# Kernel tuning notes

Hardware: AMD Instinct MI355X
Metric: run time of the kernel (lower is better)

The kernel has to match this reference:

```python
import jax, jax.numpy as jnp
import numpy as np

NUM_HEADS = 16

def setup_inputs() -> dict:
    key = jax.random.key(0)
    k1, k2, k3 = jax.random.split(key, 3)
    B, S, H = 2, 2048, 1024
    hidden_states = jax.random.normal(k1, (B, S, H), dtype=jnp.float32)
    # nn.Linear default init scale ~ 1/sqrt(fan_in); keep magnitudes sane
    w_qkv = jax.random.normal(k2, (3 * H, H), dtype=jnp.float32) * (1.0 / np.sqrt(H))
    w_o = jax.random.normal(k3, (H, H), dtype=jnp.float32) * (1.0 / np.sqrt(H))
    return {"hidden_states": hidden_states, "w_qkv": w_qkv, "w_o": w_o}

def reference(hidden_states, w_qkv, w_o):
    B, S, H = hidden_states.shape
    nh = NUM_HEADS
    hd = H // nh
    scale = 1.0 / np.sqrt(hd)
    # fused QKV projection: [B,S,3H]
    qkv = jnp.einsum('bsh,oh->bso', hidden_states, w_qkv)
    qkv = qkv.reshape(B, S, 3, nh, hd)
    q = qkv[:, :, 0].transpose(0, 2, 1, 3)  # [B, nh, S, hd]
    k = qkv[:, :, 1].transpose(0, 2, 1, 3)
    v = qkv[:, :, 2].transpose(0, 2, 1, 3)
    # scaled dot-product attention (math identical to the online-softmax path)
    scores = jnp.einsum('bhqd,bhkd->bhqk', q, k) * scale
    probs = jax.nn.softmax(scores, axis=-1)
    attn = jnp.einsum('bhqk,bhkd->bhqd', probs, v)  # [B, nh, S, hd]
    attn = attn.transpose(0, 2, 1, 3).reshape(B, S, H)
    out = jnp.einsum('bsh,oh->bso', attn, w_o)
    return out
```

## Files before the change

kernel.cpp:

```cpp
#include <hip/hip_runtime.h>

using f32x4 = __attribute__((ext_vector_type(4))) float;
using s16x8 = __attribute__((ext_vector_type(8))) short;
using u16x8 = __attribute__((ext_vector_type(8))) unsigned short;
using u16x4 = __attribute__((ext_vector_type(4))) unsigned short;
using u32x2 = __attribute__((ext_vector_type(2))) unsigned int;

__device__ __forceinline__ unsigned short f2bf(float f) {
  union { float f; unsigned u; } v; v.f = f;
  return (unsigned short)((v.u + 0x7FFFu + ((v.u >> 16) & 1u)) >> 16);
}

__device__ __forceinline__ unsigned pk2bf(float a, float b) {
#if __has_builtin(__builtin_amdgcn_cvt_pk_bf16_f32)
  typedef __bf16 bf2 __attribute__((ext_vector_type(2)));
  union { bf2 v; unsigned u; } c;
  c.v = __builtin_amdgcn_cvt_pk_bf16_f32(a, b);
  return c.u;
#else
  return (unsigned)f2bf(a) | ((unsigned)f2bf(b) << 16);
#endif
}

__device__ __forceinline__ f32x4 fzero4() {
  f32x4 z; z[0] = 0.f; z[1] = 0.f; z[2] = 0.f; z[3] = 0.f; return z;
}

__device__ __forceinline__ void gl_lds16(const void* g, void* l) {
  __builtin_amdgcn_global_load_lds(
      (const __attribute__((address_space(1))) unsigned int*)g,
      (__attribute__((address_space(3))) unsigned int*)l, 16, 0, 0);
}

__global__ __launch_bounds__(256) void cvt_bf16(const float* __restrict__ h,
                                                const float* __restrict__ wq,
                                                const float* __restrict__ wo,
                                                unsigned short* __restrict__ dst) {
  const int blk = blockIdx.x;
  const float* src;
  if (blk < 2048) src = h;
  else if (blk < 3584) src = wq - 4194304;
  else src = wo - (4194304 + 3145728);
  const size_t i = (size_t)blk * 2048 + threadIdx.x * 8;
  f32x4 a0 = *(const f32x4*)(src + i);
  f32x4 a1 = *(const f32x4*)(src + i + 4);
  u32x2 v0, v1;
  v0[0] = pk2bf(a0[0], a0[1]); v0[1] = pk2bf(a0[2], a0[3]);
  v1[0] = pk2bf(a1[0], a1[1]); v1[1] = pk2bf(a1[2], a1[3]);
  *(u32x2*)(dst + i) = v0;
  *(u32x2*)(dst + i + 4) = v1;
}

template <int CMODE>
__global__ __launch_bounds__(256) void gemm_bt(const unsigned short* __restrict__ A,
                                               const unsigned short* __restrict__ B,
                                               void* __restrict__ Cp,
                                               void* __restrict__ Vgp,
                                               int M, int N, int K) {
  __shared__ unsigned short As[128 * 64];
  __shared__ unsigned short Bs[128 * 64];
  const int t = threadIdx.x;
  const int lane = t & 63, wid = t >> 6;
  const int l15 = lane & 15, quad = lane >> 4;
  const int bm = blockIdx.x * 128, bn = blockIdx.y * 128;
  const int wm = (wid >> 1) * 64, wn = (wid & 1) * 64;
  const int wbase = t & ~63;

  f32x4 acc[4][4];
#pragma unroll
  for (int i = 0; i < 4; ++i)
#pragma unroll
    for (int j = 0; j < 4; ++j) acc[i][j] = fzero4();

  for (int k0 = 0; k0 < K; k0 += 64) {
    __syncthreads();
#pragma unroll
    for (int i = 0; i < 4; ++i) {
      const int dc = t + i * 256;
      const int row = dc >> 3, cp = dc & 7;
      const int cl = cp ^ (row & 7);
      gl_lds16(A + (size_t)(bm + row) * K + k0 + cl * 8, &As[(size_t)(i * 256 + wbase) * 8]);
      gl_lds16(B + (size_t)(bn + row) * K + k0 + cl * 8, &Bs[(size_t)(i * 256 + wbase) * 8]);
    }
    __syncthreads();
#pragma unroll
    for (int c = 0; c < 2; ++c) {
      s16x8 af[4], bf[4];
#pragma unroll
      for (int mt = 0; mt < 4; ++mt) {
        const int row = wm + mt * 16 + l15;
        af[mt] = *(const s16x8*)&As[row * 64 + (((c * 4 + quad) ^ (l15 & 7)) * 8)];
      }
#pragma unroll
      for (int nt = 0; nt < 4; ++nt) {
        const int row = wn + nt * 16 + l15;
        bf[nt] = *(const s16x8*)&Bs[row * 64 + (((c * 4 + quad) ^ (l15 & 7)) * 8)];
      }
#pragma unroll
      for (int mt = 0; mt < 4; ++mt)
#pragma unroll
        for (int nt = 0; nt < 4; ++nt)
          acc[mt][nt] = __builtin_amdgcn_mfma_f32_16x16x32_bf16(af[mt], bf[nt], acc[mt][nt], 0, 0, 0);
    }
  }

  if (CMODE == 2 && bn >= 2048) {
#pragma unroll
    for (int mt = 0; mt < 4; ++mt)
#pragma unroll
      for (int nt = 0; nt < 4; ++nt) {
        const int row0 = bm + wm + mt * 16 + quad * 4;
        const int c = bn + wn + nt * 16 + l15 - 2048;
        const int b = row0 >> 11, s = row0 & 2047;
        u32x2 ov;
        ov[0] = pk2bf(acc[mt][nt][0], acc[mt][nt][1]);
        ov[1] = pk2bf(acc[mt][nt][2], acc[mt][nt][3]);
        *(u32x2*)&((unsigned short*)Vgp)[(size_t)b * (1024 * 2048) + (size_t)c * 2048 + s] = ov;
      }
    return;
  }

  const float qscale = (CMODE == 2 && bn < 1024) ? 0.18033688011112042f : 1.0f;
#pragma unroll
  for (int mt = 0; mt < 4; ++mt)
#pragma unroll
    for (int nt = 0; nt < 4; ++nt)
#pragma unroll
      for (int r = 0; r < 4; ++r) {
        const int row = bm + wm + mt * 16 + quad * 4 + r;
        const int col = bn + wn + nt * 16 + l15;
        if (CMODE == 0)
          ((float*)Cp)[(size_t)row * N + col] = acc[mt][nt][r];
        else
          ((unsigned short*)Cp)[(size_t)row * 2048 + col] = f2bf(acc[mt][nt][r] * qscale);
      }
}

__global__ __launch_bounds__(256) void fattn(const unsigned short* __restrict__ qk,
                                             const unsigned short* __restrict__ vg,
                                             unsigned short* __restrict__ attn) {
  constexpr int S = 2048, H = 1024, LD = 2048, HD = 64;
  __shared__ unsigned short smemKP[64 * 136];
  __shared__ unsigned short Vt[64 * 128];
  unsigned short* Ks = smemKP;
  unsigned short(*Pn)[136] = (unsigned short(*)[136])smemKP;

  const int t = threadIdx.x, lane = t & 63, wid = t >> 6;
  const int l15 = lane & 15, quad = lane >> 4;
  const int qt = blockIdx.x, h = blockIdx.y, b = blockIdx.z;
  const unsigned short* qbase = qk + (size_t)b * S * LD;
  const unsigned short* vbase = vg + ((size_t)b * 16 + h) * HD * S;
  const int qrow0 = qt * 64;
  const int wbase = t & ~63;

  s16x8 qf[2];
#pragma unroll
  for (int c = 0; c < 2; ++c)
    qf[c] = *(const s16x8*)(qbase + (size_t)(qrow0 + wid * 16 + l15) * LD +
                            h * HD + c * 32 + quad * 8);

  s16x8 ones;
#pragma unroll
  for (int j = 0; j < 8; ++j) ones[j] = (short)0x3F80;

  f32x4 o[4], lacc = fzero4();
#pragma unroll
  for (int i = 0; i < 4; ++i) o[i] = fzero4();

  for (int kt = 0; kt < S / 128; ++kt) {
    __syncthreads();
#pragma unroll
    for (int i = 0; i < 4; ++i) {
      const int pos = t + i * 256;
      {
        const int row = pos >> 3, s = pos & 7;
        const int clog = s ^ (row & 7);
        gl_lds16(qbase + (size_t)(kt * 128 + row) * LD + 1024 + h * HD + clog * 8,
                 &Ks[(size_t)(i * 256 + wbase) * 8]);
      }
      {
        const int row = pos >> 4, s = pos & 15;
        const int clog = s ^ (row & 7);
        gl_lds16(vbase + (size_t)row * S + kt * 128 + clog * 8,
                 &Vt[(size_t)(i * 256 + wbase) * 8]);
      }
    }
    __syncthreads();

    f32x4 st[8];
#pragma unroll
    for (int i = 0; i < 8; ++i) st[i] = fzero4();
#pragma unroll
    for (int c = 0; c < 2; ++c)
#pragma unroll
      for (int mt = 0; mt < 8; ++mt) {
        s16x8 kf = *(const s16x8*)&Ks[(mt * 16 + l15) * 64 + ((c * 4 + quad) ^ (l15 & 7)) * 8];
        st[mt] = __builtin_amdgcn_mfma_f32_16x16x32_bf16(kf, qf[c], st[mt], 0, 0, 0);
      }

#pragma unroll
    for (int mt = 0; mt < 8; ++mt)
#pragma unroll
      for (int r = 0; r < 4; ++r) st[mt][r] = __builtin_amdgcn_exp2f(st[mt][r]);

    __syncthreads();

#pragma unroll
    for (int mt = 0; mt < 8; ++mt) {
      u32x2 pk;
      pk[0] = pk2bf(st[mt][0], st[mt][1]);
      pk[1] = pk2bf(st[mt][2], st[mt][3]);
      *(u32x2*)&Pn[wid * 16 + l15][mt * 16 + quad * 4] = pk;
    }

#pragma unroll
    for (int c = 0; c < 4; ++c) {
      s16x8 pf = *(const s16x8*)&Pn[wid * 16 + l15][c * 32 + quad * 8];
      lacc = __builtin_amdgcn_mfma_f32_16x16x32_bf16(ones, pf, lacc, 0, 0, 0);
#pragma unroll
      for (int mt = 0; mt < 4; ++mt) {
        s16x8 vf = *(const s16x8*)&Vt[(mt * 16 + l15) * 128 + (((c * 4 + quad) ^ (l15 & 7))) * 8];
        o[mt] = __builtin_amdgcn_mfma_f32_16x16x32_bf16(vf, pf, o[mt], 0, 0, 0);
      }
    }
  }

  const float inv = 1.f / lacc[0];
  const int row = b * S + qrow0 + wid * 16 + l15;
#pragma unroll
  for (int mt = 0; mt < 4; ++mt) {
    u32x2 ov;
    ov[0] = pk2bf(o[mt][0] * inv, o[mt][1] * inv);
    ov[1] = pk2bf(o[mt][2] * inv, o[mt][3] * inv);
    *(u32x2*)&attn[(size_t)row * H + h * HD + mt * 16 + quad * 4] = ov;
  }
}

extern "C" void kernel_launch(void* const* d_in, const int* in_sizes, int n_in,
                              void* d_out, int out_size, void* d_ws, size_t ws_size,
                              hipStream_t stream) {
  const float* hidden = (const float*)d_in[0];
  const float* w_qkv = (const float*)d_in[1];
  const float* w_o = (const float*)d_in[2];
  float* out = (float*)d_out;

  constexpr int B = 2, S = 2048, H = 1024;
  constexpr int M = B * S;

  unsigned short* hbf = (unsigned short*)d_ws;
  unsigned short* wqbf = hbf + 4194304;
  unsigned short* wobf = wqbf + 3145728;
  unsigned short* qkbuf = wobf + 1048576;
  unsigned short* vg = qkbuf + (size_t)M * 2048;
  unsigned short* attn = hbf;

  dim3 blk(256);
  cvt_bf16<<<4096, blk, 0, stream>>>(hidden, w_qkv, w_o, hbf);
  gemm_bt<2><<<dim3(M / 128, (3 * H) / 128), blk, 0, stream>>>(
      hbf, wqbf, (void*)qkbuf, (void*)vg, M, 3 * H, H);
  fattn<<<dim3(S / 64, 16, B), blk, 0, stream>>>(qkbuf, vg, attn);
  gemm_bt<0><<<dim3(M / 128, H / 128), blk, 0, stream>>>(
      attn, wobf, (void*)out, nullptr, M, H, H);
}
```

Baseline: 206.1 us.

## Double-buffer K/V tiles and process 32 query rows per wave in attention

```diff
diff --git a/kernel.cpp b/kernel.cpp
--- a/kernel.cpp
+++ b/kernel.cpp
@@ -140,99 +140,127 @@
                                              const unsigned short* __restrict__ vg,
                                              unsigned short* __restrict__ attn) {
   constexpr int S = 2048, H = 1024, LD = 2048, HD = 64;
-  __shared__ unsigned short smemKP[64 * 136];
-  __shared__ unsigned short Vt[64 * 128];
-  unsigned short* Ks = smemKP;
-  unsigned short(*Pn)[136] = (unsigned short(*)[136])smemKP;
+  __shared__ unsigned short Ks[2][64 * 64];
+  __shared__ unsigned short Vt[2][64 * 64];
+  __shared__ unsigned short Pn[4][32][72];
 
   const int t = threadIdx.x, lane = t & 63, wid = t >> 6;
   const int l15 = lane & 15, quad = lane >> 4;
   const int qt = blockIdx.x, h = blockIdx.y, b = blockIdx.z;
   const unsigned short* qbase = qk + (size_t)b * S * LD;
+  const unsigned short* kbase = qbase + 1024 + h * HD;
   const unsigned short* vbase = vg + ((size_t)b * 16 + h) * HD * S;
-  const int qrow0 = qt * 64;
+  const int qrow0 = qt * 128;
   const int wbase = t & ~63;
 
-  s16x8 qf[2];
-#pragma unroll
-  for (int c = 0; c < 2; ++c)
-    qf[c] = *(const s16x8*)(qbase + (size_t)(qrow0 + wid * 16 + l15) * LD +
-                            h * HD + c * 32 + quad * 8);
+  s16x8 qf[2][2];
+#pragma unroll
+  for (int nt = 0; nt < 2; ++nt)
+#pragma unroll
+    for (int c = 0; c < 2; ++c)
+      qf[nt][c] = *(const s16x8*)(qbase + (size_t)(qrow0 + wid * 32 + nt * 16 + l15) * LD +
+                                  h * HD + c * 32 + quad * 8);
 
   s16x8 ones;
 #pragma unroll
   for (int j = 0; j < 8; ++j) ones[j] = (short)0x3F80;
 
-  f32x4 o[4], lacc = fzero4();
-#pragma unroll
-  for (int i = 0; i < 4; ++i) o[i] = fzero4();
-
-  for (int kt = 0; kt < S / 128; ++kt) {
+  f32x4 o[4][2], lacc[2];
+#pragma unroll
+  for (int i = 0; i < 4; ++i)
+#pragma unroll
+    for (int j = 0; j < 2; ++j) o[i][j] = fzero4();
+  lacc[0] = fzero4(); lacc[1] = fzero4();
+
+  auto stage = [&](int kt, int bu) {
+#pragma unroll
+    for (int i = 0; i < 2; ++i) {
+      const int pos = t + i * 256;
+      const int row = pos >> 3, s = pos & 7;
+      const int clog = s ^ (row & 7);
+      gl_lds16(kbase + (size_t)(kt * 64 + row) * LD + clog * 8,
+               &Ks[bu][(size_t)(i * 256 + wbase) * 8]);
+      gl_lds16(vbase + (size_t)row * S + kt * 64 + clog * 8,
+               &Vt[bu][(size_t)(i * 256 + wbase) * 8]);
+    }
+  };
+
+  stage(0, 0);
+  __syncthreads();
+
+  for (int kt = 0; kt < S / 64; ++kt) {
+    const int cur = kt & 1;
+    if (kt < S / 64 - 1) stage(kt + 1, cur ^ 1);
+
+    const unsigned short* K = Ks[cur];
+    const unsigned short* V = Vt[cur];
+
+    f32x4 st[4][2];
+#pragma unroll
+    for (int i = 0; i < 4; ++i)
+#pragma unroll
+      for (int j = 0; j < 2; ++j) st[i][j] = fzero4();
+#pragma unroll
+    for (int c = 0; c < 2; ++c) {
+      s16x8 kf[4];
+#pragma unroll
+      for (int mt = 0; mt < 4; ++mt)
+        kf[mt] = *(const s16x8*)&K[(mt * 16 + l15) * 64 + ((c * 4 + quad) ^ (l15 & 7)) * 8];
+#pragma unroll
+      for (int mt = 0; mt < 4; ++mt)
+#pragma unroll
+        for (int nt = 0; nt < 2; ++nt)
+          st[mt][nt] = __builtin_amdgcn_mfma_f32_16x16x32_bf16(kf[mt], qf[nt][c], st[mt][nt], 0, 0, 0);
+    }
+
+#pragma unroll
+    for (int mt = 0; mt < 4; ++mt)
+#pragma unroll
+      for (int nt = 0; nt < 2; ++nt)
+#pragma unroll
+        for (int r = 0; r < 4; ++r) st[mt][nt][r] = __builtin_amdgcn_exp2f(st[mt][nt][r]);
+
+#pragma unroll
+    for (int mt = 0; mt < 4; ++mt)
+#pragma unroll
+      for (int nt = 0; nt < 2; ++nt) {
+        u32x2 pk;
+        pk[0] = pk2bf(st[mt][nt][0], st[mt][nt][1]);
+        pk[1] = pk2bf(st[mt][nt][2], st[mt][nt][3]);
+        *(u32x2*)&Pn[wid][nt * 16 + l15][mt * 16 + quad * 4] = pk;
+      }
+
+#pragma unroll
+    for (int c = 0; c < 2; ++c) {
+      s16x8 pf[2];
+#pragma unroll
+      for (int nt = 0; nt < 2; ++nt) {
+        pf[nt] = *(const s16x8*)&Pn[wid][nt * 16 + l15][c * 32 + quad * 8];
+        lacc[nt] = __builtin_amdgcn_mfma_f32_16x16x32_bf16(ones, pf[nt], lacc[nt], 0, 0, 0);
+      }
+#pragma unroll
+      for (int mt = 0; mt < 4; ++mt) {
+        s16x8 vf = *(const s16x8*)&V[(mt * 16 + l15) * 64 + ((c * 4 + quad) ^ (l15 & 7)) * 8];
+#pragma unroll
+        for (int nt = 0; nt < 2; ++nt)
+          o[mt][nt] = __builtin_amdgcn_mfma_f32_16x16x32_bf16(vf, pf[nt], o[mt][nt], 0, 0, 0);
+      }
+    }
+
     __syncthreads();
-#pragma unroll
-    for (int i = 0; i < 4; ++i) {
-      const int pos = t + i * 256;
-      {
-        const int row = pos >> 3, s = pos & 7;
-        const int clog = s ^ (row & 7);
-        gl_lds16(qbase + (size_t)(kt * 128 + row) * LD + 1024 + h * HD + clog * 8,
-                 &Ks[(size_t)(i * 256 + wbase) * 8]);
-      }
-      {
-        const int row = pos >> 4, s = pos & 15;
-        const int clog = s ^ (row & 7);
-        gl_lds16(vbase + (size_t)row * S + kt * 128 + clog * 8,
-                 &Vt[(size_t)(i * 256 + wbase) * 8]);
-      }
-    }
-    __syncthreads();
-
-    f32x4 st[8];
-#pragma unroll
-    for (int i = 0; i < 8; ++i) st[i] = fzero4();
-#pragma unroll
-    for (int c = 0; c < 2; ++c)
-#pragma unroll
-      for (int mt = 0; mt < 8; ++mt) {
-        s16x8 kf = *(const s16x8*)&Ks[(mt * 16 + l15) * 64 + ((c * 4 + quad) ^ (l15 & 7)) * 8];
-        st[mt] = __builtin_amdgcn_mfma_f32_16x16x32_bf16(kf, qf[c], st[mt], 0, 0, 0);
-      }
-
-#pragma unroll
-    for (int mt = 0; mt < 8; ++mt)
-#pragma unroll
-      for (int r = 0; r < 4; ++r) st[mt][r] = __builtin_amdgcn_exp2f(st[mt][r]);
-
-    __syncthreads();
-
-#pragma unroll
-    for (int mt = 0; mt < 8; ++mt) {
-      u32x2 pk;
-      pk[0] = pk2bf(st[mt][0], st[mt][1]);
-      pk[1] = pk2bf(st[mt][2], st[mt][3]);
-      *(u32x2*)&Pn[wid * 16 + l15][mt * 16 + quad * 4] = pk;
-    }
-
-#pragma unroll
-    for (int c = 0; c < 4; ++c) {
-      s16x8 pf = *(const s16x8*)&Pn[wid * 16 + l15][c * 32 + quad * 8];
-      lacc = __builtin_amdgcn_mfma_f32_16x16x32_bf16(ones, pf, lacc, 0, 0, 0);
-#pragma unroll
-      for (int mt = 0; mt < 4; ++mt) {
-        s16x8 vf = *(const s16x8*)&Vt[(mt * 16 + l15) * 128 + (((c * 4 + quad) ^ (l15 & 7))) * 8];
-        o[mt] = __builtin_amdgcn_mfma_f32_16x16x32_bf16(vf, pf, o[mt], 0, 0, 0);
-      }
-    }
-  }
-
-  const float inv = 1.f / lacc[0];
-  const int row = b * S + qrow0 + wid * 16 + l15;
-#pragma unroll
-  for (int mt = 0; mt < 4; ++mt) {
-    u32x2 ov;
-    ov[0] = pk2bf(o[mt][0] * inv, o[mt][1] * inv);
-    ov[1] = pk2bf(o[mt][2] * inv, o[mt][3] * inv);
-    *(u32x2*)&attn[(size_t)row * H + h * HD + mt * 16 + quad * 4] = ov;
+  }
+
+#pragma unroll
+  for (int nt = 0; nt < 2; ++nt) {
+    const float inv = 1.f / lacc[nt][0];
+    const int row = b * S + qrow0 + wid * 32 + nt * 16 + l15;
+#pragma unroll
+    for (int mt = 0; mt < 4; ++mt) {
+      u32x2 ov;
+      ov[0] = pk2bf(o[mt][nt][0] * inv, o[mt][nt][1] * inv);
+      ov[1] = pk2bf(o[mt][nt][2] * inv, o[mt][nt][3] * inv);
+      *(u32x2*)&attn[(size_t)row * H + h * HD + mt * 16 + quad * 4] = ov;
+    }
   }
 }
 
@@ -258,7 +286,7 @@
   cvt_bf16<<<4096, blk, 0, stream>>>(hidden, w_qkv, w_o, hbf);
   gemm_bt<2><<<dim3(M / 128, (3 * H) / 128), blk, 0, stream>>>(
       hbf, wqbf, (void*)qkbuf, (void*)vg, M, 3 * H, H);
-  fattn<<<dim3(S / 64, 16, B), blk, 0, stream>>>(qkbuf, vg, attn);
+  fattn<<<dim3(S / 128, 16, B), blk, 0, stream>>>(qkbuf, vg, attn);
   gemm_bt<0><<<dim3(M / 128, H / 128), blk, 0, stream>>>(
       attn, wobf, (void*)out, nullptr, M, H, H);
 }
```

New measurement: 187.6 us. -9.0%, faster.
